# Kernel tuning notes

Hardware: AMD Instinct MI355X
Metric: run time of the kernel (lower is better)

## Reference

```python
import jax, jax.numpy as jnp
import numpy as np

C = 256; M = 8; K = 4; L = 4; DFF = 1024; CV = C // M
SHAPES = [(100, 100), (50, 50), (25, 25), (13, 13)]
B = 16; LQ = 900


def setup_inputs() -> dict:
    key = jax.random.key(0)
    ks = iter(jax.random.split(key, 64))
    def n(shape, s=0.02):
        return jax.random.normal(next(ks), shape, jnp.float32) * s
    inp = {
        "query_objects": n((LQ, B, C), 1.0),
        "query_poses": n((LQ, B, C), 1.0),
        "ref_points": jax.random.uniform(next(ks), (LQ, B, 2), jnp.float32),
    }
    for i, (h, w) in enumerate(SHAPES):
        inp[f"feat{i}"] = n((B, h, w, C), 1.0)
        inp[f"pos{i}"] = n((B, h, w, C), 1.0)
    inp.update(dict(
        sa_in_w=n((C, 3 * C)), sa_in_b=jnp.zeros((3 * C,), jnp.float32),
        sa_out_w=n((C, C)), sa_out_b=jnp.zeros((C,), jnp.float32),
        n1_g=jnp.ones((C,), jnp.float32), n1_b=jnp.zeros((C,), jnp.float32),
        n2_g=jnp.ones((C,), jnp.float32), n2_b=jnp.zeros((C,), jnp.float32),
        n3_g=jnp.ones((C,), jnp.float32), n3_b=jnp.zeros((C,), jnp.float32),
        val_w=n((C, C)), val_b=jnp.zeros((C,), jnp.float32),
        off_w=n((C, M * L * K * 2)), off_b=n((M * L * K * 2,), 0.5),
        aw_w=n((C, M * L * K)), aw_b=jnp.zeros((M * L * K,), jnp.float32),
        dout_w=n((C, C)), dout_b=jnp.zeros((C,), jnp.float32),
        ffn_w1=n((C, DFF)), ffn_b1=jnp.zeros((DFF,), jnp.float32),
        ffn_w2=n((DFF, C)), ffn_b2=jnp.zeros((C,), jnp.float32),
    ))
    return inp


def layernorm(x, g, b, eps=1e-5):
    m = x.mean(-1, keepdims=True)
    v = ((x - m) ** 2).mean(-1, keepdims=True)
    return (x - m) * jax.lax.rsqrt(v + eps) * g + b


def mha(x_q, x_k, x_v, Win, bin_, Wout, bout):
    # torch nn.MultiheadAttention, seq-first (Lq, B, C), no masks, eval mode
    Lq, Bn, _ = x_q.shape
    q = (x_q @ Win[:, :C] + bin_[:C]).reshape(Lq, Bn, M, CV)
    k = (x_k @ Win[:, C:2 * C] + bin_[C:2 * C]).reshape(Lq, Bn, M, CV)
    v = (x_v @ Win[:, 2 * C:] + bin_[2 * C:]).reshape(Lq, Bn, M, CV)
    a = jax.nn.softmax(jnp.einsum('qbmd,kbmd->bmqk', q * (CV ** -0.5), k), axis=-1)
    o = jnp.einsum('bmqk,kbmd->qbmd', a, v).reshape(Lq, Bn, C)
    return o @ Wout + bout


def deform_attn(qd, ref, feats, val_w, val_b, off_w, off_b, aw_w, aw_b, dout_w, dout_b):
    # qd: (B, Lq, C) queries; ref: (B, Lq, 2) normalized [0,1] reference points (x, y)
    Bn, Lq, _ = qd.shape
    off = (qd @ off_w + off_b).reshape(Bn, Lq, M, L, K, 2)            # sampling offsets (pixels)
    aw = jax.nn.softmax((qd @ aw_w + aw_b).reshape(Bn, Lq, M, L * K), axis=-1)
    aw = aw.reshape(Bn, Lq, M, L, K)                                   # attention weights over L*K
    out = jnp.zeros((Bn, Lq, M, CV), qd.dtype)
    for l, feat in enumerate(feats):
        H, W = feat.shape[1], feat.shape[2]
        # shared value projection, split into heads: (B, M, HW, Cv)
        v = (feat.reshape(Bn, H * W, C) @ val_w + val_b).reshape(Bn, H * W, M, CV).transpose(0, 2, 1, 3)
        px = ref[:, :, None, None, 0] * W - 0.5 + off[:, :, :, l, :, 0]  # (B, Lq, M, K)
        py = ref[:, :, None, None, 1] * H - 0.5 + off[:, :, :, l, :, 1]
        x0 = jnp.floor(px); y0 = jnp.floor(py)
        samp = jnp.zeros((Bn, M, Lq, K, CV), qd.dtype)
        for dx in (0.0, 1.0):
            for dy in (0.0, 1.0):
                xi = x0 + dx; yi = y0 + dy
                wgt = (1.0 - jnp.abs(px - xi)) * (1.0 - jnp.abs(py - yi))
                valid = (xi >= 0) & (xi < W) & (yi >= 0) & (yi < H)      # zero padding outside
                idx = (jnp.clip(yi, 0, H - 1) * W + jnp.clip(xi, 0, W - 1)).astype(jnp.int32)
                idx_t = idx.transpose(0, 2, 1, 3).reshape(Bn, M, Lq * K)
                g = jnp.take_along_axis(v, idx_t[..., None], axis=2).reshape(Bn, M, Lq, K, CV)
                samp = samp + g * (wgt * valid).transpose(0, 2, 1, 3)[..., None]
        out = out + jnp.einsum('bqmk,bmqkc->bqmc', aw[:, :, :, l], samp)
    return out.reshape(Bn, Lq, C) @ dout_w + dout_b


def reference(query_objects, query_poses, ref_points, feat0, feat1, feat2, feat3,
              pos0, pos1, pos2, pos3, sa_in_w, sa_in_b, sa_out_w, sa_out_b,
              n1_g, n1_b, n2_g, n2_b, n3_g, n3_b, val_w, val_b, off_w, off_b,
              aw_w, aw_b, dout_w, dout_b, ffn_w1, ffn_b1, ffn_w2, ffn_b2):
    # post-norm decoder layer, eval mode (dropout = identity)
    q = query_objects + query_poses
    x = query_objects + mha(q, q, query_objects, sa_in_w, sa_in_b, sa_out_w, sa_out_b)
    x = layernorm(x, n1_g, n1_b)
    feats = [feat0 + pos0, feat1 + pos1, feat2 + pos2, feat3 + pos3]
    qd = x.transpose(1, 0, 2)              # (B, Lq, C)
    ref = ref_points.transpose(1, 0, 2)    # (B, Lq, 2)
    d = deform_attn(qd, ref, feats, val_w, val_b, off_w, off_b, aw_w, aw_b, dout_w, dout_b)
    x = x + d.transpose(1, 0, 2)
    x = layernorm(x, n2_g, n2_b)
    x = x + (jax.nn.relu(x @ ffn_w1 + ffn_b1) @ ffn_w2 + ffn_b2)
    x = layernorm(x, n3_g, n3_b)
    return x
```

## Files before the change

### kernel.cpp

```cpp
#include <hip/hip_runtime.h>
#include <hip/hip_bf16.h>
#include <cstdint>

#define LQ 900
#define BB 16
#define CC 256
#define MM 8
#define CV 32
#define NROWS (LQ * BB)

typedef __attribute__((ext_vector_type(8))) short short8;
typedef __attribute__((ext_vector_type(4))) float f32x4;

__device__ __forceinline__ short f2bf(float f) {
    union { float f; unsigned u; } x; x.f = f;
    const unsigned r = x.u + 0x7fff + ((x.u >> 16) & 1);
    return (short)(r >> 16);
}
__device__ __forceinline__ float bf2f(ushort u) {
    union { unsigned u; float f; } c; c.u = ((unsigned)u) << 16; return c.f;
}

__device__ __constant__ int d_HW[4]    = {100, 50, 25, 13};
__device__ __constant__ int d_baseR[4] = {0, 160000, 200000, 210000};

__global__ __launch_bounds__(256) void conv_w_T(
    const float* __restrict__ W, ushort* __restrict__ Wt, int K, int N)
{
    __shared__ float tl[32][33];
    const int t = threadIdx.x;
    const int tx = t & 31, ty = t >> 5;
    const int n0 = blockIdx.x * 32, k0 = blockIdx.y * 32;
    #pragma unroll
    for (int p = 0; p < 4; ++p)
        tl[ty + 8 * p][tx] = W[(size_t)(k0 + ty + 8 * p) * N + n0 + tx];
    __syncthreads();
    #pragma unroll
    for (int p = 0; p < 4; ++p)
        Wt[(size_t)(n0 + ty + 8 * p) * K + k0 + tx] = (ushort)f2bf(tl[tx][ty + 8 * p]);
}

__global__ void concat_bias(const float* __restrict__ a, const float* __restrict__ b,
                            float* __restrict__ o)
{
    const int t = blockIdx.x * 256 + threadIdx.x;
    if (t < 384) o[t] = (t < 256) ? a[t] : b[t - 256];
}

#define EPS 136
#define LDSN 17408

template<bool A_BF16, bool ADD_A2, bool RELU, bool RESID, bool OUT_BF16>
__device__ __forceinline__ void gemm_core(
    ushort* lds,
    const void* __restrict__ Ap, const float* __restrict__ A2, int lda,
    const ushort* __restrict__ Bt, const float* __restrict__ bias,
    const float* __restrict__ resid, void* __restrict__ Cp, int ldc,
    int Mr, int Kd, int row0, int col0)
{
    ushort* As = lds;
    ushort* Bs = lds + 8192;

    const int t = threadIdx.x;
    const int lane = t & 63;
    const int w = t >> 6;
    const int wr = w >> 1, wc = w & 1;
    const int lr = lane & 15, lk = lane >> 4;

    f32x4 acc[4][4] = {};

    const int srow = t >> 4;
    const int skq  = (t & 15) * 4;
    const int sg   = (t & 15) >> 1;
    const int srem = (t & 1) * 8;

    const float*  Af = (const float*)Ap;
    const ushort* Ah = (const ushort*)Ap;

    short4 sa_[8], sb_[8];
    float4 fa_[8], f2_[8];

    const int nk = Kd >> 6;

    auto issue = [&](int kk0) {
        #pragma unroll
        for (int p = 0; p < 8; ++p) {
            const int gr = min(row0 + p * 16 + srow, Mr - 1);
            if constexpr (A_BF16) {
                sa_[p] = *reinterpret_cast<const short4*>(Ah + (size_t)gr * lda + kk0 + skq);
            } else {
                fa_[p] = *reinterpret_cast<const float4*>(Af + (size_t)gr * lda + kk0 + skq);
                if constexpr (ADD_A2)
                    f2_[p] = *reinterpret_cast<const float4*>(A2 + (size_t)gr * lda + kk0 + skq);
            }
            sb_[p] = *reinterpret_cast<const short4*>(Bt + (size_t)(col0 + p * 16 + srow) * Kd + kk0 + skq);
        }
    };

    issue(0);

    for (int kt = 0; kt < nk; ++kt) {
        #pragma unroll
        for (int p = 0; p < 8; ++p) {
            const int r = p * 16 + srow;
            short4 a4;
            if constexpr (A_BF16) {
                a4 = sa_[p];
            } else {
                float4 av = fa_[p];
                if constexpr (ADD_A2) {
                    av.x += f2_[p].x; av.y += f2_[p].y; av.z += f2_[p].z; av.w += f2_[p].w;
                }
                a4.x = f2bf(av.x); a4.y = f2bf(av.y); a4.z = f2bf(av.z); a4.w = f2bf(av.w);
            }
            const int byteA = r * 128 + ((sg ^ (r & 7)) << 4) + srem;
            *reinterpret_cast<short4*>((char*)As + byteA) = a4;
            *reinterpret_cast<short4*>((char*)Bs + byteA) = sb_[p];
        }
        __syncthreads();

        if (kt + 1 < nk) issue((kt + 1) * 64);

        #pragma unroll
        for (int kk = 0; kk < 2; ++kk) {
            short8 af[4], bfr[4];
            #pragma unroll
            for (int i = 0; i < 4; ++i) {
                const int r = wr * 64 + i * 16 + lr;
                const int byte = r * 128 + (((kk * 4 + lk) ^ (r & 7)) << 4);
                af[i] = *reinterpret_cast<const short8*>((char*)As + byte);
            }
            #pragma unroll
            for (int j = 0; j < 4; ++j) {
                const int r = wc * 64 + j * 16 + lr;
                const int byte = r * 128 + (((kk * 4 + lk) ^ (r & 7)) << 4);
                bfr[j] = *reinterpret_cast<const short8*>((char*)Bs + byte);
            }
            #pragma unroll
            for (int i = 0; i < 4; ++i)
                #pragma unroll
                for (int j = 0; j < 4; ++j)
                    acc[i][j] = __builtin_amdgcn_mfma_f32_16x16x32_bf16(af[i], bfr[j], acc[i][j], 0, 0, 0);
        }
        __syncthreads();
    }

    if constexpr (OUT_BF16) {
        ushort* Cb = (ushort*)Cp;
        #pragma unroll
        for (int j = 0; j < 4; ++j) {
            const int lcol = wc * 64 + j * 16 + lr;
            const float bcol = bias[col0 + lcol];
            #pragma unroll
            for (int i = 0; i < 4; ++i) {
                const int lrbase = wr * 64 + i * 16 + lk * 4;
                #pragma unroll
                for (int reg = 0; reg < 4; ++reg) {
                    float v = acc[i][j][reg] + bcol;
                    if (RELU) v = fmaxf(v, 0.f);
                    lds[(lrbase + reg) * EPS + lcol] = (ushort)f2bf(v);
                }
            }
        }
        __syncthreads();
        const int erow = t >> 1, ehalf = t & 1;
        if (row0 + erow < Mr) {
            ushort* dst = Cb + (size_t)(row0 + erow) * ldc + col0 + ehalf * 64;
            const ushort* src = lds + erow * EPS + ehalf * 64;
            #pragma unroll
            for (int q = 0; q < 8; ++q)
                *reinterpret_cast<short8*>(dst + q * 8) =
                    *reinterpret_cast<const short8*>(src + q * 8);
        }
    } else {
        float* Cf = (float*)Cp;
        #pragma unroll
        for (int j = 0; j < 4; ++j) {
            const int col = col0 + wc * 64 + j * 16 + lr;
            const float bcol = bias[col];
            #pragma unroll
            for (int i = 0; i < 4; ++i) {
                const int rbase = row0 + wr * 64 + i * 16 + lk * 4;
                #pragma unroll
                for (int reg = 0; reg < 4; ++reg) {
                    const int r = rbase + reg;
                    if (r < Mr) {
                        float v = acc[i][j][reg] + bcol;
                        if (RESID) v += resid[(size_t)r * ldc + col];
                        if (RELU)  v = fmaxf(v, 0.f);
                        Cf[(size_t)r * ldc + col] = v;
                    }
                }
            }
        }
    }
}

template<bool A_BF16, bool ADD_A2, bool RELU, bool RESID, bool OUT_BF16>
__global__ __launch_bounds__(256) void gemm_bf16(
    const void* __restrict__ Ap, const float* __restrict__ A2, int lda,
    const ushort* __restrict__ Bt, const float* __restrict__ bias,
    const float* __restrict__ resid, void* __restrict__ Cp, int ldc,
    int Mr, int Kd)
{
    __shared__ ushort lds[LDSN];
    gemm_core<A_BF16, ADD_A2, RELU, RESID, OUT_BF16>(
        lds, Ap, A2, lda, Bt, bias, resid, Cp, ldc, Mr, Kd,
        blockIdx.y * 128, blockIdx.x * 128);
}

__global__ __launch_bounds__(256) void val_gemm(
    const float* __restrict__ f0, const float* __restrict__ p0,
    const float* __restrict__ f1, const float* __restrict__ p1,
    const float* __restrict__ f2, const float* __restrict__ p2,
    const float* __restrict__ f3, const float* __restrict__ p3,
    const ushort* __restrict__ Bt, const float* __restrict__ bias,
    ushort* __restrict__ Vval)
{
    __shared__ ushort lds[LDSN];
    int by = blockIdx.y;
    const float *Af, *A2;
    int Mr, obase;
    if (by < 1250)      { Af = f0; A2 = p0; Mr = 160000; obase = 0;      }
    else if (by < 1563) { Af = f1; A2 = p1; Mr = 40000;  obase = 160000; by -= 1250; }
    else if (by < 1642) { Af = f2; A2 = p2; Mr = 10000;  obase = 200000; by -= 1563; }
    else                { Af = f3; A2 = p3; Mr = 2704;   obase = 210000; by -= 1642; }
    gemm_core<false, true, false, false, true>(
        lds, Af, A2, 256, Bt, bias, nullptr,
        Vval + (size_t)obase * 256, 256, Mr, 256, by * 128, blockIdx.x * 128);
}

__global__ __launch_bounds__(256) void attn_mfma(
    const ushort* __restrict__ QKbf, const ushort* __restrict__ Vbf,
    ushort* __restrict__ attnO)
{
    __shared__ ushort K_lds[64][40];
    __shared__ ushort Vt[32][72];
    __shared__ ushort P_lds[4][16][72];

    const int t = threadIdx.x;
    const int w = t >> 6, lane = t & 63;
    const int q0 = blockIdx.x * 64;
    const int m = blockIdx.y & 7, b = blockIdx.y >> 3;

    const int lr = lane & 15;
    const int lk = lane >> 4;

    const int qrow = min(q0 + w * 16 + lr, LQ - 1);
    const short8 qf = *reinterpret_cast<const short8*>(
        QKbf + ((size_t)qrow * BB + b) * 512 + m * 32 + lk * 8);

    f32x4 oacc[2] = {f32x4{0.f,0.f,0.f,0.f}, f32x4{0.f,0.f,0.f,0.f}};
    float mrun[4] = {-1e30f, -1e30f, -1e30f, -1e30f};
    float lrun[4] = {0.f, 0.f, 0.f, 0.f};

    const float scale = 0.17677669529663687f;
    const int sr = t >> 2;
    const int sd = (t & 3) * 8;

    for (int k0 = 0; k0 < LQ; k0 += 64) {
        {
            const int kr = min(k0 + sr, LQ - 1);
            *reinterpret_cast<short8*>(&K_lds[sr][sd]) =
                *reinterpret_cast<const short8*>(QKbf + ((size_t)kr * BB + b) * 512 + 256 + m * 32 + sd);
            const short8 v8 = *reinterpret_cast<const short8*>(
                Vbf + ((size_t)kr * BB + b) * 256 + m * 32 + sd);
            #pragma unroll
            for (int j = 0; j < 8; ++j) Vt[sd + j][sr] = (ushort)v8[j];
        }
        __syncthreads();

        f32x4 sa[4];
        #pragma unroll
        for (int n = 0; n < 4; ++n) {
            const short8 kf = *reinterpret_cast<const short8*>(&K_lds[n * 16 + lr][lk * 8]);
            sa[n] = __builtin_amdgcn_mfma_f32_16x16x32_bf16(qf, kf, f32x4{0.f,0.f,0.f,0.f}, 0, 0, 0);
        }
        #pragma unroll
        for (int n = 0; n < 4; ++n)
            #pragma unroll
            for (int r = 0; r < 4; ++r)
                sa[n][r] *= scale;
        if (k0 + 64 > LQ) {
            #pragma unroll
            for (int n = 0; n < 4; ++n)
                if (k0 + n * 16 + lr >= LQ) {
                    #pragma unroll
                    for (int r = 0; r < 4; ++r) sa[n][r] = -1e30f;
                }
        }

        #pragma unroll
        for (int r = 0; r < 4; ++r) {
            float mx = fmaxf(fmaxf(sa[0][r], sa[1][r]), fmaxf(sa[2][r], sa[3][r]));
            #pragma unroll
            for (int o = 8; o; o >>= 1) mx = fmaxf(mx, __shfl_xor(mx, o));
            const float mnew = fmaxf(mrun[r], mx);
            const float corr = __expf(mrun[r] - mnew);
            mrun[r] = mnew;
            float psum = 0.f;
            #pragma unroll
            for (int n = 0; n < 4; ++n) {
                const float p = __expf(sa[n][r] - mnew);
                psum += p;
                P_lds[w][lk * 4 + r][n * 16 + lr] = (ushort)f2bf(p);
            }
            #pragma unroll
            for (int o = 8; o; o >>= 1) psum += __shfl_xor(psum, o);
            lrun[r] = lrun[r] * corr + psum;
            oacc[0][r] *= corr;
            oacc[1][r] *= corr;
        }

        #pragma unroll
        for (int kk = 0; kk < 2; ++kk) {
            const short8 pf = *reinterpret_cast<const short8*>(&P_lds[w][lr][kk * 32 + lk * 8]);
            #pragma unroll
            for (int dt = 0; dt < 2; ++dt) {
                const short8 vf = *reinterpret_cast<const short8*>(&Vt[dt * 16 + lr][kk * 32 + lk * 8]);
                oacc[dt] = __builtin_amdgcn_mfma_f32_16x16x32_bf16(pf, vf, oacc[dt], 0, 0, 0);
            }
        }
        __syncthreads();
    }

    #pragma unroll
    for (int r = 0; r < 4; ++r) {
        const int row = q0 + w * 16 + lk * 4 + r;
        if (row < LQ) {
            const float inv = 1.f / lrun[r];
            ushort* op = attnO + ((size_t)row * BB + b) * 256 + m * 32;
            op[lr]      = (ushort)f2bf(oacc[0][r] * inv);
            op[16 + lr] = (ushort)f2bf(oacc[1][r] * inv);
        }
    }
}

__global__ __launch_bounds__(256) void ln_kernel(
    const float* __restrict__ X, const float* __restrict__ g,
    const float* __restrict__ bta, float* __restrict__ Y, int nrows)
{
    const int r = blockIdx.x * 4 + (threadIdx.x >> 6);
    if (r >= nrows) return;
    const int lane = threadIdx.x & 63;
    const float4 v = *reinterpret_cast<const float4*>(X + (size_t)r * 256 + lane * 4);
    float s  = v.x + v.y + v.z + v.w;
    float sq = v.x * v.x + v.y * v.y + v.z * v.z + v.w * v.w;
    #pragma unroll
    for (int o = 32; o; o >>= 1) { s += __shfl_xor(s, o); sq += __shfl_xor(sq, o); }
    const float mean = s * (1.f / 256.f);
    const float var  = sq * (1.f / 256.f) - mean * mean;
    const float rs   = rsqrtf(var + 1e-5f);
    const float4 gv = *reinterpret_cast<const float4*>(g + lane * 4);
    const float4 bv = *reinterpret_cast<const float4*>(bta + lane * 4);
    float4 o4;
    o4.x = (v.x - mean) * rs * gv.x + bv.x;
    o4.y = (v.y - mean) * rs * gv.y + bv.y;
    o4.z = (v.z - mean) * rs * gv.z + bv.z;
    o4.w = (v.w - mean) * rs * gv.w + bv.w;
    *reinterpret_cast<float4*>(Y + (size_t)r * 256 + lane * 4) = o4;
}

__global__ __launch_bounds__(256) void samp_prep(
    const float* __restrict__ ref, const float* __restrict__ obf,
    int4* __restrict__ prepI, float4* __restrict__ prepW)
{
    const int gid = blockIdx.x * 256 + threadIdx.x;
    const int k = gid & 3, l = (gid >> 2) & 3, m = (gid >> 4) & 7, row = gid >> 7;
    const int b = row & 15;

    const float logit = obf[(size_t)row * 384 + 256 + m * 16 + l * 4 + k];
    float mx = logit;
    #pragma unroll
    for (int o = 1; o < 16; o <<= 1) mx = fmaxf(mx, __shfl_xor(mx, o));
    const float e = __expf(logit - mx);
    float se = e;
    #pragma unroll
    for (int o = 1; o < 16; o <<= 1) se += __shfl_xor(se, o);
    const float aw = e / se;

    const int   Hl = d_HW[l];
    const float Hf = (float)Hl;
    const int   gbase = d_baseR[l] + b * Hl * Hl;
    const float rx = ref[row * 2 + 0], ry = ref[row * 2 + 1];
    const float ox = obf[(size_t)row * 384 + m * 32 + l * 8 + k * 2 + 0];
    const float oy = obf[(size_t)row * 384 + m * 32 + l * 8 + k * 2 + 1];
    const float px = rx * Hf - 0.5f + ox;
    const float py = ry * Hf - 0.5f + oy;
    const float x0 = floorf(px), y0 = floorf(py);

    int4 I; float4 W;
    #pragma unroll
    for (int c = 0; c < 4; ++c) {
        const float xi = x0 + (float)(c & 1);
        const float yi = y0 + (float)(c >> 1);
        const float wv = (1.f - fabsf(px - xi)) * (1.f - fabsf(py - yi));
        const bool valid = (xi >= 0.f) && (xi < Hf) && (yi >= 0.f) && (yi < Hf);
        const int ix = min(max((int)xi, 0), Hl - 1);
        const int iy = min(max((int)yi, 0), Hl - 1);
        const int idx = gbase + iy * Hl + ix;
        const float wgt = valid ? aw * wv : 0.f;
        if (c == 0) { I.x = idx; W.x = wgt; }
        else if (c == 1) { I.y = idx; W.y = wgt; }
        else if (c == 2) { I.z = idx; W.z = wgt; }
        else { I.w = idx; W.w = wgt; }
    }
    prepI[gid] = I;
    prepW[gid] = W;
}

__global__ __launch_bounds__(256) void samp_gather(
    const ushort* __restrict__ Vval, const int4* __restrict__ prepI,
    const float4* __restrict__ prepW, float* __restrict__ samp)
{
    const int wid  = blockIdx.x * 4 + (threadIdx.x >> 6);
    const int lane = threadIdx.x & 63;
    const int q  = wid % LQ;
    const int bm = wid / LQ;
    const int m  = bm & 7, b = bm >> 3;
    const int row = q * BB + b;
    const int sid = lane >> 3, dg = lane & 7;

    const uint2* V4 = (const uint2*)Vval;
    const int pbase = (row * 8 + m) * 16;
    const int coff  = m * 8 + dg;

    float a0 = 0.f, a1 = 0.f, a2 = 0.f, a3 = 0.f;
    #pragma unroll
    for (int g = 0; g < 2; ++g) {
        const int s = g * 8 + sid;
        const int4   I = prepI[pbase + s];
        const float4 W = prepW[pbase + s];
        uint2 v;
        v = V4[(size_t)I.x * 64 + coff];
        a0 += W.x * bf2f((ushort)v.x); a1 += W.x * bf2f((ushort)(v.x >> 16));
        a2 += W.x * bf2f((ushort)v.y); a3 += W.x * bf2f((ushort)(v.y >> 16));
        v = V4[(size_t)I.y * 64 + coff];
        a0 += W.y * bf2f((ushort)v.x); a1 += W.y * bf2f((ushort)(v.x >> 16));
        a2 += W.y * bf2f((ushort)v.y); a3 += W.y * bf2f((ushort)(v.y >> 16));
        v = V4[(size_t)I.z * 64 + coff];
        a0 += W.z * bf2f((ushort)v.x); a1 += W.z * bf2f((ushort)(v.x >> 16));
        a2 += W.z * bf2f((ushort)v.y); a3 += W.z * bf2f((ushort)(v.y >> 16));
        v = V4[(size_t)I.w * 64 + coff];
        a0 += W.w * bf2f((ushort)v.x); a1 += W.w * bf2f((ushort)(v.x >> 16));
        a2 += W.w * bf2f((ushort)v.y); a3 += W.w * bf2f((ushort)(v.y >> 16));
    }
    #pragma unroll
    for (int o = 8; o <= 32; o <<= 1) {
        a0 += __shfl_xor(a0, o); a1 += __shfl_xor(a1, o);
        a2 += __shfl_xor(a2, o); a3 += __shfl_xor(a3, o);
    }
    if (sid == 0) {
        float4 o4; o4.x = a0; o4.y = a1; o4.z = a2; o4.w = a3;
        *reinterpret_cast<float4*>(samp + (size_t)row * 256 + m * 32 + dg * 4) = o4;
    }
}

extern "C" void kernel_launch(void* const* d_in, const int* in_sizes, int n_in,
                              void* d_out, int out_size, void* d_ws, size_t ws_size,
                              hipStream_t stream)
{
    const float* qo   = (const float*)d_in[0];
    const float* qpz  = (const float*)d_in[1];
    const float* refp = (const float*)d_in[2];
    const float* feat[4] = {(const float*)d_in[3], (const float*)d_in[5],
                            (const float*)d_in[7], (const float*)d_in[9]};
    const float* pos[4]  = {(const float*)d_in[4], (const float*)d_in[6],
                            (const float*)d_in[8], (const float*)d_in[10]};
    const float* sa_in_w  = (const float*)d_in[11];
    const float* sa_in_b  = (const float*)d_in[12];
    const float* sa_out_w = (const float*)d_in[13];
    const float* sa_out_b = (const float*)d_in[14];
    const float* n1_g = (const float*)d_in[15];
    const float* n1_b = (const float*)d_in[16];
    const float* n2_g = (const float*)d_in[17];
    const float* n2_b = (const float*)d_in[18];
    const float* n3_g = (const float*)d_in[19];
    const float* n3_b = (const float*)d_in[20];
    const float* val_w  = (const float*)d_in[21];
    const float* val_b  = (const float*)d_in[22];
    const float* off_w  = (const float*)d_in[23];
    const float* off_b  = (const float*)d_in[24];
    const float* aw_w   = (const float*)d_in[25];
    const float* aw_b   = (const float*)d_in[26];
    const float* dout_w = (const float*)d_in[27];
    const float* dout_b = (const float*)d_in[28];
    const float* ffn_w1 = (const float*)d_in[29];
    const float* ffn_b1 = (const float*)d_in[30];
    const float* ffn_w2 = (const float*)d_in[31];
    const float* ffn_b2 = (const float*)d_in[32];

    char* ws = (char*)d_ws;
    ushort* QKbf   = (ushort*)(ws + 0);
    ushort* Vbf    = (ushort*)(ws + 14745600);
    ushort* attnO  = (ushort*)(ws + 22118400);
    ushort* Vval   = (ushort*)(ws + 29491200);
    ushort* WsaInT = (ushort*)(ws + 138395648);
    ushort* WsaOutT= (ushort*)(ws + 138788864);
    ushort* WvalT  = (ushort*)(ws + 138919936);
    ushort* WdoutT = (ushort*)(ws + 139051008);
    ushort* Wffn1T = (ushort*)(ws + 139182080);
    ushort* Wffn2T = (ushort*)(ws + 139706368);
    ushort* WoffAwT= (ushort*)(ws + 140230656);
    float*  obias  = (float*)(ws + 140427264);
    float* x1   = (float*)(ws + 140429312);
    float* dres = x1;
    float* xln1 = (float*)(ws + 155174912);
    float* obf  = (float*)(ws + 169920512);
    float* x3   = obf;
    float* samp = (float*)(ws + 192038912);
    float* xln2 = (float*)(ws + 206784512);
    ushort* h   = (ushort*)(ws + 221530112);
    int4*  prepI = (int4*)(ws + 251021312);
    float4* prepW = (float4*)(ws + 280512512);

    const dim3 blk(256);
    const int GM = (NROWS + 127) / 128;

    conv_w_T<<<dim3(24, 8), blk, 0, stream>>>(sa_in_w, WsaInT, 256, 768);
    conv_w_T<<<dim3(8, 8), blk, 0, stream>>>(sa_out_w, WsaOutT, 256, 256);
    conv_w_T<<<dim3(8, 8), blk, 0, stream>>>(val_w, WvalT, 256, 256);
    conv_w_T<<<dim3(8, 8), blk, 0, stream>>>(dout_w, WdoutT, 256, 256);
    conv_w_T<<<dim3(32, 8), blk, 0, stream>>>(ffn_w1, Wffn1T, 256, 1024);
    conv_w_T<<<dim3(8, 32), blk, 0, stream>>>(ffn_w2, Wffn2T, 1024, 256);
    conv_w_T<<<dim3(8, 8), blk, 0, stream>>>(off_w, WoffAwT, 256, 256);
    conv_w_T<<<dim3(4, 8), blk, 0, stream>>>(aw_w, WoffAwT + 256 * 256, 256, 128);
    concat_bias<<<dim3(2), blk, 0, stream>>>(off_b, aw_b, obias);

    gemm_bf16<false, true, false, false, true><<<dim3(4, GM), blk, 0, stream>>>(
        qo, qpz, 256, WsaInT, sa_in_b, nullptr, QKbf, 512, NROWS, 256);
    gemm_bf16<false, false, false, false, true><<<dim3(2, GM), blk, 0, stream>>>(
        qo, nullptr, 256, WsaInT + 512 * 256, sa_in_b + 512, nullptr, Vbf, 256, NROWS, 256);
    attn_mfma<<<dim3(15, 128), blk, 0, stream>>>(QKbf, Vbf, attnO);
    gemm_bf16<true, false, false, true, false><<<dim3(2, GM), blk, 0, stream>>>(
        attnO, nullptr, 256, WsaOutT, sa_out_b, qo, x1, 256, NROWS, 256);
    ln_kernel<<<dim3(3600), blk, 0, stream>>>(x1, n1_g, n1_b, xln1, NROWS);
    gemm_bf16<false, false, false, false, false><<<dim3(3, GM), blk, 0, stream>>>(
        xln1, nullptr, 256, WoffAwT, obias, nullptr, obf, 384, NROWS, 256);
    samp_prep<<<dim3(7200), blk, 0, stream>>>(refp, obf, prepI, prepW);
    val_gemm<<<dim3(2, 1664), blk, 0, stream>>>(
        feat[0], pos[0], feat[1], pos[1], feat[2], pos[2], feat[3], pos[3],
        WvalT, val_b, Vval);
    samp_gather<<<dim3(28800), blk, 0, stream>>>(Vval, prepI, prepW, samp);
    gemm_bf16<false, false, false, true, false><<<dim3(2, GM), blk, 0, stream>>>(
        samp, nullptr, 256, WdoutT, dout_b, xln1, dres, 256, NROWS, 256);
    ln_kernel<<<dim3(3600), blk, 0, stream>>>(dres, n2_g, n2_b, xln2, NROWS);
    gemm_bf16<false, false, true, false, true><<<dim3(8, GM), blk, 0, stream>>>(
        xln2, nullptr, 256, Wffn1T, ffn_b1, nullptr, h, 1024, NROWS, 256);
    gemm_bf16<true, false, false, true, false><<<dim3(2, GM), blk, 0, stream>>>(
        h, nullptr, 1024, Wffn2T, ffn_b2, xln2, x3, 256, NROWS, 1024);
    ln_kernel<<<dim3(3600), blk, 0, stream>>>(x3, n3_g, n3_b, (float*)d_out, NROWS);
}
```

Before: 606.6 us.

## Rewrite value projection as persistent kernel with full weight matrix resident in LDS

Replaces the tiled value GEMM over the four feature levels with a persistent kernel of 256 blocks of 768 threads. Each block loads the whole 256x256 bf16 weight matrix into LDS once, using an XOR swizzle, plus the bias. Each wave then processes 16-row tiles, streaming feat+pos straight from global memory into MFMA B fragments with register prefetch. This removes the repeated per-tile weight staging and the A-tile LDS round-trips. In exchange it needs about 130KB of LDS per block, which limits occupancy to one block per CU, and relies on the hard-coded static tile distribution.

```diff
diff --git a/kernel.cpp b/kernel.cpp
--- a/kernel.cpp
+++ b/kernel.cpp
@@ -209,25 +209,91 @@
         blockIdx.y * 128, blockIdx.x * 128);
 }
 
-__global__ __launch_bounds__(256) void val_gemm(
+#define VAL_TILES 13294
+
+__global__ __launch_bounds__(768) void val_gemm3(
     const float* __restrict__ f0, const float* __restrict__ p0,
     const float* __restrict__ f1, const float* __restrict__ p1,
     const float* __restrict__ f2, const float* __restrict__ p2,
     const float* __restrict__ f3, const float* __restrict__ p3,
-    const ushort* __restrict__ Bt, const float* __restrict__ bias,
+    const ushort* __restrict__ Wt, const float* __restrict__ bias,
     ushort* __restrict__ Vval)
 {
-    __shared__ ushort lds[LDSN];
-    int by = blockIdx.y;
-    const float *Af, *A2;
-    int Mr, obase;
-    if (by < 1250)      { Af = f0; A2 = p0; Mr = 160000; obase = 0;      }
-    else if (by < 1563) { Af = f1; A2 = p1; Mr = 40000;  obase = 160000; by -= 1250; }
-    else if (by < 1642) { Af = f2; A2 = p2; Mr = 10000;  obase = 200000; by -= 1563; }
-    else                { Af = f3; A2 = p3; Mr = 2704;   obase = 210000; by -= 1642; }
-    gemm_core<false, true, false, false, true>(
-        lds, Af, A2, 256, Bt, bias, nullptr,
-        Vval + (size_t)obase * 256, 256, Mr, 256, by * 128, blockIdx.x * 128);
+    __shared__ ushort wlds[66048];
+    float* blds = (float*)(wlds + 65536);
+
+    const int t = threadIdx.x;
+    for (int c = t; c < 16384; c += 768) {
+        const int h = c & 1, g = (c >> 1) & 7, r = (c >> 4) & 255, k64 = c >> 12;
+        const int dst = k64 * 32768 + r * 128 + ((g ^ (r & 7)) << 4) + h * 8;
+        const short4 v = *reinterpret_cast<const short4*>(
+            Wt + (size_t)r * 256 + k64 * 64 + g * 8 + h * 4);
+        *reinterpret_cast<short4*>((char*)wlds + dst) = v;
+    }
+    if (t < 256) blds[t] = bias[t];
+    __syncthreads();
+
+    const int w = t >> 6, lane = t & 63;
+    const int lr = lane & 15, lk = lane >> 4;
+    const int wg = blockIdx.x * 12 + w;
+    int tile  = wg * 4 + min(wg, 1006);
+    int count = (wg < 1006) ? 5 : 4;
+
+    for (; count > 0; --count, ++tile) {
+        const float *fb, *pb; int lrow;
+        if (tile < 10000)      { fb = f0; pb = p0; lrow = tile * 16; }
+        else if (tile < 12500) { fb = f1; pb = p1; lrow = (tile - 10000) * 16; }
+        else if (tile < 13125) { fb = f2; pb = p2; lrow = (tile - 12500) * 16; }
+        else                   { fb = f3; pb = p3; lrow = (tile - 13125) * 16; }
+        const float* fA = fb + (size_t)(lrow + lr) * 256 + lk * 8;
+        const float* pA = pb + (size_t)(lrow + lr) * 256 + lk * 8;
+
+        f32x4 acc[16];
+        #pragma unroll
+        for (int nt = 0; nt < 16; ++nt) acc[nt] = f32x4{0.f, 0.f, 0.f, 0.f};
+
+        float4 cf0 = *reinterpret_cast<const float4*>(fA);
+        float4 cf1 = *reinterpret_cast<const float4*>(fA + 4);
+        float4 cp0 = *reinterpret_cast<const float4*>(pA);
+        float4 cp1 = *reinterpret_cast<const float4*>(pA + 4);
+        #pragma unroll
+        for (int kt = 0; kt < 8; ++kt) {
+            float4 nf0, nf1, np0, np1;
+            if (kt < 7) {
+                nf0 = *reinterpret_cast<const float4*>(fA + (kt + 1) * 32);
+                nf1 = *reinterpret_cast<const float4*>(fA + (kt + 1) * 32 + 4);
+                np0 = *reinterpret_cast<const float4*>(pA + (kt + 1) * 32);
+                np1 = *reinterpret_cast<const float4*>(pA + (kt + 1) * 32 + 4);
+            }
+            short8 bfrag;
+            bfrag[0] = f2bf(cf0.x + cp0.x); bfrag[1] = f2bf(cf0.y + cp0.y);
+            bfrag[2] = f2bf(cf0.z + cp0.z); bfrag[3] = f2bf(cf0.w + cp0.w);
+            bfrag[4] = f2bf(cf1.x + cp1.x); bfrag[5] = f2bf(cf1.y + cp1.y);
+            bfrag[6] = f2bf(cf1.z + cp1.z); bfrag[7] = f2bf(cf1.w + cp1.w);
+            const int kbase = (kt >> 1) * 32768;
+            const int gsh = (kt & 1) * 4 + lk;
+            #pragma unroll
+            for (int nt = 0; nt < 16; ++nt) {
+                const int r = nt * 16 + lr;
+                const int byte = kbase + r * 128 + ((gsh ^ (r & 7)) << 4);
+                const short8 wf = *reinterpret_cast<const short8*>((char*)wlds + byte);
+                acc[nt] = __builtin_amdgcn_mfma_f32_16x16x32_bf16(wf, bfrag, acc[nt], 0, 0, 0);
+            }
+            cf0 = nf0; cf1 = nf1; cp0 = np0; cp1 = np1;
+        }
+
+        ushort* orow = Vval + (size_t)(tile * 16 + lr) * 256 + lk * 4;
+        #pragma unroll
+        for (int nt = 0; nt < 16; ++nt) {
+            const float4 b4 = *reinterpret_cast<const float4*>(&blds[nt * 16 + lk * 4]);
+            short4 u;
+            u.x = f2bf(acc[nt][0] + b4.x);
+            u.y = f2bf(acc[nt][1] + b4.y);
+            u.z = f2bf(acc[nt][2] + b4.z);
+            u.w = f2bf(acc[nt][3] + b4.w);
+            *reinterpret_cast<short4*>(orow + nt * 16) = u;
+        }
+    }
 }
 
 __global__ __launch_bounds__(256) void attn_mfma(
@@ -538,7 +604,7 @@
     gemm_bf16<false, false, false, false, false><<<dim3(3, GM), blk, 0, stream>>>(
         xln1, nullptr, 256, WoffAwT, obias, nullptr, obf, 384, NROWS, 256);
     samp_prep<<<dim3(7200), blk, 0, stream>>>(refp, obf, prepI, prepW);
-    val_gemm<<<dim3(2, 1664), blk, 0, stream>>>(
+    val_gemm3<<<dim3(256), dim3(768), 0, stream>>>(
         feat[0], pos[0], feat[1], pos[1], feat[2], pos[2], feat[3], pos[3],
         WvalT, val_b, Vval);
     samp_gather<<<dim3(28800), blk, 0, stream>>>(Vval, prepI, prepW, samp);
```

After: 1.071 ms. 1.77x slower.
